# Performance work log

Hardware: AMD Instinct MI355X
Metric: run time of the kernel (lower is better)

Reference implementation:

```python
import jax, jax.numpy as jnp
import numpy as np

K, NC, NA = 9, 13, 5
NB, NH, NW = 128, 26, 26
NT, L = 50, 2 * K + 3
NOOBJ, OBJ, SIL = 1.0, 5.0, 0.6
COORD_S, CLASS_S = 1.0, 1.0
PRETRAIN_EPOCHS = 15
TH, SHARP = 80.0, 2.0                      # corner-conf distance threshold (px), sharpness
SCALE = np.array([640.0, 480.0], np.float32)  # im_width, im_height used by corner_confidences
CONF0 = float(np.exp(SHARP) - 1.0)
ANCHORS = np.array([1.482, 2.2412, 2.0501, 3.1265, 2.3946, 4.6891,
                    3.1018, 3.991, 3.4879, 5.8851], np.float32).reshape(NA, 2)


def setup_inputs():
    k1, k2 = jax.random.split(jax.random.key(0))
    output = jax.random.normal(k1, (NB, NA * (2 * K + 1 + NC), NH, NW), dtype=jnp.float32)
    target = jax.random.uniform(k2, (NB, NT * L), dtype=jnp.float32)
    return {"output": output, "target": target, "epoch": 20}


def _corner_conf(pred, gt):
    # pred, gt: [..., K, 2] normalized corners -> mean per-corner confidence [...]
    d = jnp.sqrt((((pred - gt) * jnp.asarray(SCALE)) ** 2).sum(-1))  # pixel distance [..., K]
    c = (jnp.exp(SHARP * (1.0 - d / TH)) - 1.0) / CONF0
    return jnp.where(d < TH, c, 0.0).mean(-1)


def _region_loss(output, target, epoch):
    nAnch, nPix = NA * NH * NW, NH * NW
    tgt = jax.lax.stop_gradient(target).reshape(NB, NT, L)
    out = output.reshape(NB, NA, 2 * K + 1 + NC, NH, NW)
    # keypoint 0 gets sigmoid, the rest are raw offsets
    xs = jnp.concatenate([jax.nn.sigmoid(out[:, :, 0:1]), out[:, :, 2:2 * K:2]], axis=2)  # [B,A,K,H,W]
    ys = jnp.concatenate([jax.nn.sigmoid(out[:, :, 1:2]), out[:, :, 3:2 * K:2]], axis=2)
    conf = jax.nn.sigmoid(out[:, :, 2 * K])                             # [B,A,H,W]
    cls_logits = jnp.transpose(out[:, :, 2 * K + 1:], (0, 1, 3, 4, 2))  # [B,A,H,W,NC]

    gxg = jnp.arange(NW, dtype=jnp.float32)
    gyg = jnp.arange(NH, dtype=jnp.float32)
    px = (jax.lax.stop_gradient(xs) + gxg) / NW            # detached, as torch uses .data
    py = (jax.lax.stop_gradient(ys) + gyg[:, None]) / NH
    # pred corners per anchor cell, flat anchor index = a*H*W + j*W + i -> [B, A*H*W, K, 2]
    pc = jnp.transpose(jnp.stack([px, py], -1), (0, 1, 3, 4, 2, 5)).reshape(NB, nAnch, K, 2)

    gt_xy = tgt[:, :, 1:1 + 2 * K].reshape(NB, NT, K, 2)
    # torch loop breaks at first target with x1 == 0 -> cumulative validity
    valid = jnp.cumprod((tgt[:, :, 1] != 0).astype(jnp.int32), axis=1) > 0  # [B,T]

    # pass 1: max corner confidence over valid GT, per anchor cell
    def max_conf_step(cur, inp):
        gt_t, v_t = inp                                    # [B,K,2], [B]
        c = _corner_conf(pc, gt_t[:, None]).reshape(NB, NA, NH, NW)
        return jnp.where(v_t[:, None, None, None], jnp.maximum(cur, c), cur), None

    cur_confs, _ = jax.lax.scan(max_conf_step, jnp.zeros((NB, NA, NH, NW), jnp.float32),
                                (jnp.swapaxes(gt_xy, 0, 1), valid.T))
    conf_mask0 = jnp.where(cur_confs > SIL, 0.0, NOOBJ)

    # per-target quantities (vectorized over b,t)
    gx = gt_xy[..., 0] * NW                                # [B,T,K]
    gy = gt_xy[..., 1] * NH
    gi0 = jnp.clip(jnp.floor(gx[:, :, 0]).astype(jnp.int32), 0, NW - 1)  # [B,T]
    gj0 = jnp.clip(jnp.floor(gy[:, :, 0]).astype(jnp.int32), 0, NH - 1)
    # pred_box is fetched with best_n == -1 (as in the source); emulate torch negative flat index via mod
    flat_idx = jnp.mod(jnp.arange(NB)[:, None] * nAnch - nPix + gj0 * NW + gi0, NB * nAnch)
    pred_box = pc.reshape(NB * nAnch, K, 2)[flat_idx]      # [B,T,K,2]
    conf_t = _corner_conf(pred_box, gt_xy)                 # [B,T]
    gw = tgt[:, :, L - 2] * NW
    gh = tgt[:, :, L - 1] * NH
    aw, ah = ANCHORS[:, 0], ANCHORS[:, 1]
    mw = jnp.minimum(aw, gw[..., None])                    # centered-box IoU (bbox_iou, cxcywh)
    mh = jnp.minimum(ah, gh[..., None])
    inter = mw * mh
    iou = inter / (aw * ah + (gw * gh)[..., None] - inter)
    best_n = jnp.argmax(iou, axis=-1).astype(jnp.int32)    # [B,T] (first max, like strict '>')
    txv = gx - gi0[..., None].astype(jnp.float32)          # [B,T,K]
    tyv = gy - gj0[..., None].astype(jnp.float32)
    tclsv = tgt[:, :, 0]

    # pass 2: sequential scatter matching torch overwrite order over t
    barange = jnp.arange(NB)
    z = jnp.zeros((NB, NA, NH, NW), jnp.float32)
    zk = jnp.zeros((NB, NA, NH, NW, K), jnp.float32)

    def scatter_step(carry, inp):
        cm, clm, cfm, tx, ty, tcf, tcl = carry
        v, bn, gj, gi, cft, txt, tyt, tct = inp
        idx = (barange, bn, gj, gi)
        vk = v[:, None]
        cm = cm.at[idx].set(jnp.where(v, 1.0, cm[idx]))
        clm = clm.at[idx].set(jnp.where(v, 1.0, clm[idx]))
        cfm = cfm.at[idx].set(jnp.where(v, OBJ, cfm[idx]))
        tx = tx.at[idx].set(jnp.where(vk, txt, tx[idx]))
        ty = ty.at[idx].set(jnp.where(vk, tyt, ty[idx]))
        tcf = tcf.at[idx].set(jnp.where(v, cft, tcf[idx]))
        tcl = tcl.at[idx].set(jnp.where(v, tct, tcl[idx]))
        return (cm, clm, cfm, tx, ty, tcf, tcl), None

    inps = (valid.T, best_n.T, gj0.T, gi0.T, conf_t.T,
            jnp.swapaxes(txv, 0, 1), jnp.swapaxes(tyv, 0, 1), tclsv.T)
    (coord_mask, cls_mask, conf_mask, tx, ty, tconf, tcls), _ = jax.lax.scan(
        scatter_step, (z, z, conf_mask0, zk, zk, z, z), inps)

    # losses
    xsT = jnp.transpose(xs, (0, 1, 3, 4, 2))               # [B,A,H,W,K]
    ysT = jnp.transpose(ys, (0, 1, 3, 4, 2))
    cmk = coord_mask[..., None]
    loss_x = 0.5 * COORD_S * jnp.sum(((xsT - tx) * cmk) ** 2)
    loss_y = 0.5 * COORD_S * jnp.sum(((ysT - ty) * cmk) ** 2)
    sq = jnp.sqrt(conf_mask)
    loss_conf = 0.5 * jnp.sum(((conf - tconf) * sq) ** 2)
    labels = jnp.clip(tcls.astype(jnp.int32), 0, NC - 1)
    ce = -jnp.take_along_axis(jax.nn.log_softmax(cls_logits, axis=-1),
                              labels[..., None], axis=-1)[..., 0]
    loss_cls = CLASS_S * jnp.sum(ce * cls_mask)
    loss = loss_x + loss_y + loss_cls
    if epoch > PRETRAIN_EPOCHS:
        loss = loss + loss_conf
    return loss


def reference(output, target, epoch):
    return _region_loss(output, target, epoch)
```

## Files before the change

kernel.cpp:

```cpp
#include <hip/hip_runtime.h>
#include <math.h>
#include <stdint.h>

#define KK     9
#define NCLS   13
#define NANC   5
#define NBB    128
#define NHH    26
#define NWW    26
#define NTT    50
#define LL     21
#define CHC    32
#define NPIX   676
#define NANCHT 3380
#define NCELLT 432640
#define GTS    20
#define MWPB   106
#define GTH_W  12
#define NBLKX  53

#define LOG2E_F   1.4426950408889634f
#define K1C       2.8853900817779268f
#define K2C       0.036067376022224085f
#define SXW       24.615384615384617f
#define SYH       18.461538461538463f
#define THRESH_S  43.500902934225507f
#define CONF_T_SCALE 0.017390849194407297f
#define OBJ_W     5.0f
#define EPOCH_PRETRAIN 15
#define BIGV      6.0e18f

#define CULL_H2   0.36f
#define HSCALE    0.03125f

typedef __attribute__((ext_vector_type(2))) float f2;
typedef __attribute__((ext_vector_type(2))) _Float16 h2;
typedef __attribute__((ext_vector_type(4))) unsigned int u4;
typedef __attribute__((ext_vector_type(2))) unsigned int u2;

static __device__ __forceinline__ float fast_exp2(float x){
  return __builtin_amdgcn_exp2f(x);
}
static __device__ __forceinline__ float fast_sqrt(float x){
  return __builtin_amdgcn_sqrtf(x);
}
static __device__ __forceinline__ float sigmoidf_(float x){
  return 1.0f/(1.0f + fast_exp2(-LOG2E_F*x));
}

__constant__ float c_anch[10] = {1.482f,2.2412f,2.0501f,3.1265f,2.3946f,4.6891f,
                                 3.1018f,3.991f,3.4879f,5.8851f};


__global__ __launch_bounds__(64) void prep_kernel(const float* __restrict__ tgt,
                                                  float* __restrict__ gts_neg,
                                                  unsigned int* __restrict__ gth,
                                                  int* __restrict__ nvalid){
  int b = blockIdx.x;
  int t = threadIdx.x;
  const float* trow = tgt + (size_t)b*NTT*LL;
  float v1 = (t < NTT) ? trow[t*LL + 1] : 0.0f;
  unsigned long long mk = __ballot(t < NTT && v1 != 0.0f);
  int firstInvalid = __ffsll(~mk) - 1;
  if (t == 0) nvalid[b] = firstInvalid;
  for (int idx = t; idx < NTT*GTS; idx += 64){
    int tt = idx / GTS;
    int c  = idx - tt*GTS;
    float v;
    if (c == 9 || c == 19)      v = BIGV;
    else if (c < 9)             v = -(trow[tt*LL + 1 + 2*c] * 640.0f);
    else                        v = -(trow[tt*LL + 2 + 2*(c-10)] * 480.0f);
    gts_neg[(size_t)b*NTT*GTS + idx] = v;
  }
  for (int idx = t; idx < NTT*GTH_W; idx += 64){
    int tt = idx / GTH_W;
    int w  = idx - tt*GTH_W;
    const float* tr2 = trow + tt*LL;
    float a0 = BIGV, a1 = BIGV;
    if (w < 5){
      int k0 = 2*w;
      a0 = -(tr2[1 + 2*k0] * 20.0f);
      if (k0 + 1 < KK) a1 = -(tr2[1 + 2*(k0+1)] * 20.0f);
    } else if (w < 10){
      int k0 = 2*(w-5);
      a0 = -(tr2[2 + 2*k0] * 15.0f);
      if (k0 + 1 < KK) a1 = -(tr2[2 + 2*(k0+1)] * 15.0f);
    }
    h2 hh; hh.x = (_Float16)a0; hh.y = (_Float16)a1;
    gth[(size_t)b*NTT*GTH_W + idx] = __builtin_bit_cast(unsigned int, hh);
  }
}

__global__ __launch_bounds__(256) void region_confmask_kernel(
    const float* __restrict__ outp, const float* __restrict__ gts_neg,
    const unsigned int* __restrict__ gth,
    const int* __restrict__ nvalid, unsigned int* __restrict__ maskw,
    double* __restrict__ partials){
  int b    = blockIdx.y;
  int lane = threadIdx.x & 63;
  int w    = threadIdx.x >> 6;
  int cellbase = blockIdx.x * 64;
  int cell = cellbase + lane;
  bool live = (cell < NANCHT);
  int cellc = live ? cell : (NANCHT-1);

  __shared__ unsigned int sgh[NTT*GTH_W] __attribute__((aligned(16)));
  __shared__ float sgt[NTT*GTS] __attribute__((aligned(16)));
  __shared__ unsigned long long sexcl[4];
  {
    const unsigned int* gsrc = gth + (size_t)b*NTT*GTH_W;
    for (int idx = threadIdx.x; idx < NTT*GTH_W; idx += 256) sgh[idx] = gsrc[idx];
    const float* fsrc = gts_neg + (size_t)b*NTT*GTS;
    for (int idx = threadIdx.x; idx < NTT*GTS; idx += 256) sgt[idx] = fsrc[idx];
  }
  __syncthreads();

  int a   = cellc / NPIX;
  int rem = cellc - a*NPIX;
  int j   = rem / NWW;
  int i   = rem - j*NWW;
  const float* base = outp + (((size_t)b*NANC + a)*CHC)*NPIX + rem;

  f2 Pxp[5], Pyp[5];
#pragma unroll
  for (int k = 0; k < KK; ++k){
    float rx = base[(2*k)*NPIX];
    float ry = base[(2*k+1)*NPIX];
    if (k == 0){ rx = sigmoidf_(rx); ry = sigmoidf_(ry); }
    Pxp[k>>1][k&1] = (rx + (float)i) * SXW;
    Pyp[k>>1][k&1] = (ry + (float)j) * SYH;
  }
  Pxp[4][1] = 0.0f; Pyp[4][1] = 0.0f;

  h2 Pxh[5], Pyh[5];
#pragma unroll
  for (int p = 0; p < 5; ++p){
    Pxh[p].x = (_Float16)(Pxp[p].x * HSCALE);
    Pxh[p].y = (_Float16)(Pxp[p].y * HSCALE);
    Pyh[p].x = (_Float16)(Pyp[p].x * HSCALE);
    Pyh[p].y = (_Float16)(Pyp[p].y * HSCALE);
  }

  int nv = nvalid[b];
  int t0 = (w*nv) >> 2;
  int t1 = ((w+1)*nv) >> 2;
  const _Float16 thh = (_Float16)CULL_H2;
  unsigned long long qbits = 0ull;
#pragma unroll 2
  for (int t = t0; t < t1; ++t){
    const u4* q = (const u4*)(sgh + t*GTH_W);
    u4 q0 = q[0];
    u4 q1 = q[1];
    u2 q2 = *(const u2*)(sgh + t*GTH_W + 8);
    h2 Xa[5] = { __builtin_bit_cast(h2, q0.x), __builtin_bit_cast(h2, q0.y),
                 __builtin_bit_cast(h2, q0.z), __builtin_bit_cast(h2, q0.w),
                 __builtin_bit_cast(h2, q1.x) };
    h2 Ya[5] = { __builtin_bit_cast(h2, q1.y), __builtin_bit_cast(h2, q1.z),
                 __builtin_bit_cast(h2, q1.w), __builtin_bit_cast(h2, q2.x),
                 __builtin_bit_cast(h2, q2.y) };
    h2 m2 = {(_Float16)60000.0f, (_Float16)60000.0f};
#pragma unroll
    for (int p = 0; p < 5; ++p){
      h2 dx = Pxh[p] + Xa[p];
      h2 dy = Pyh[p] + Ya[p];
      h2 r  = __builtin_elementwise_fma(dy, dy, dx*dx);
      m2 = __builtin_elementwise_min(m2, r);
    }
    _Float16 mm = (m2.x < m2.y) ? m2.x : m2.y;
    if (mm < thh) qbits |= (1ull << t);
  }

  bool exc = false;
  if (__any(qbits != 0ull)){
    while (qbits){
      int t = __ffsll((long long)qbits) - 1;
      qbits &= qbits - 1;
      const float* gg = sgt + t*GTS;
      float s = 0.0f;
#pragma unroll
      for (int k = 0; k < KK; ++k){
        float dx = Pxp[k>>1][k&1] + gg[k];
        float dy = Pyp[k>>1][k&1] + gg[10+k];
        float d  = fast_sqrt(fmaf(dy, dy, dx*dx));
        float e  = fast_exp2(fmaf(d, -K2C, K1C));
        s += fmaxf(e, 1.0f);
      }
      exc |= (s > THRESH_S);
    }
  }

  unsigned long long em = __ballot(exc);
  if (lane == 0) sexcl[w] = em;
  __syncthreads();

  if (w == 0){
    unsigned long long finalx = sexcl[0] | sexcl[1] | sexcl[2] | sexcl[3];
    int m0 = ((finalx >> lane) & 1ull) ? 0 : 1;

    float cf = sigmoidf_(base[(2*KK)*NPIX]);
    float contrib = (m0 && live) ? 0.5f*cf*cf : 0.0f;

    unsigned long long mb = __ballot(m0 != 0);
    if ((lane & 31) == 0){
      unsigned int wv = (lane == 0) ? (unsigned int)mb : (unsigned int)(mb >> 32);
      maskw[(size_t)b*MWPB + (cellbase >> 5) + (lane >> 5)] = wv;
    }

#pragma unroll
    for (int o = 32; o > 0; o >>= 1) contrib += __shfl_xor(contrib, o, 64);
    if (lane == 0)
      partials[(size_t)b*NBLKX + blockIdx.x] = (double)contrib;
  }
}

__global__ __launch_bounds__(64) void scatter_loss_kernel(
    const float* __restrict__ outp, const float* __restrict__ tgt,
    const int* __restrict__ nvalid, const unsigned int* __restrict__ maskw,
    double* __restrict__ bc_part){
  int b = blockIdx.x;
  int t = threadIdx.x;
  __shared__ int keys[NTT];
  int nv = nvalid[b];
  bool valid = (t < nv);

  int key = -1, gi0 = 0, gj0 = 0, bn = 0;
  float txv[KK], tyv[KK];
  float conf_t = 0.0f, tcls = 0.0f;

  if (t < NTT){
    const float* trow = tgt + ((size_t)b*NTT + t)*LL;
    tcls = trow[0];
    float gx0 = trow[1]*(float)NWW;
    float gy0 = trow[2]*(float)NHH;
    gi0 = min(max((int)floorf(gx0), 0), NWW-1);
    gj0 = min(max((int)floorf(gy0), 0), NHH-1);
#pragma unroll
    for (int k = 0; k < KK; ++k){
      txv[k] = trow[1+2*k]*(float)NWW - (float)gi0;
      tyv[k] = trow[2+2*k]*(float)NHH - (float)gj0;
    }
    float gw = trow[LL-2]*(float)NWW, gh = trow[LL-1]*(float)NHH;
    float best = -1.0f;
    for (int a = 0; a < NANC; ++a){
      float aw = c_anch[2*a], ah = c_anch[2*a+1];
      float inter = fminf(aw, gw) * fminf(ah, gh);
      float iou = inter / (aw*ah + gw*gh - inter);
      if (iou > best){ best = iou; bn = a; }
    }
    key = bn*NPIX + gj0*NWW + gi0;
    keys[t] = key;

    long f = (long)b*NANCHT - NPIX + gj0*NWW + gi0;
    if (f < 0) f += NCELLT;
    int bb  = (int)(f / NANCHT);
    int rr  = (int)(f - (long)bb*NANCHT);
    int aa  = rr / NPIX;
    int rr2 = rr - aa*NPIX;
    int jj  = rr2 / NWW;
    int ii  = rr2 - jj*NWW;
    const float* pbase = outp + (((size_t)bb*NANC + aa)*CHC)*NPIX + rr2;
    float s = 0.0f;
#pragma unroll
    for (int k = 0; k < KK; ++k){
      float rx = pbase[(2*k)*NPIX], ry = pbase[(2*k+1)*NPIX];
      if (k == 0){ rx = sigmoidf_(rx); ry = sigmoidf_(ry); }
      float Pxx = (rx + (float)ii)*SXW, Pyy = (ry + (float)jj)*SYH;
      float dx = Pxx - trow[1+2*k]*640.0f;
      float dy = Pyy - trow[2+2*k]*480.0f;
      float d  = fast_sqrt(fmaf(dy, dy, dx*dx));
      float e  = fast_exp2(fmaf(d, -K2C, K1C));
      s += fmaxf(e, 1.0f);
    }
    conf_t = (s - 9.0f) * CONF_T_SCALE;
  }
  __syncthreads();

  bool winner = valid;
  if (valid){
    for (int u = t+1; u < nv; ++u) if (keys[u] == key){ winner = false; break; }
  }

  double lx = 0.0, ly = 0.0, lcls = 0.0, lcf = 0.0;
  if (winner){
    const float* cbase = outp + (((size_t)b*NANC + bn)*CHC)*NPIX + gj0*NWW + gi0;
    float sx = 0.0f, sy = 0.0f;
#pragma unroll
    for (int k = 0; k < KK; ++k){
      float rx = cbase[(2*k)*NPIX], ry = cbase[(2*k+1)*NPIX];
      if (k == 0){ rx = sigmoidf_(rx); ry = sigmoidf_(ry); }
      float dx = rx - txv[k], dy = ry - tyv[k];
      sx = fmaf(dx, dx, sx); sy = fmaf(dy, dy, sy);
    }
    lx = 0.5*(double)sx; ly = 0.5*(double)sy;

    float lg[NCLS], mx = -1e30f;
#pragma unroll
    for (int c = 0; c < NCLS; ++c){ lg[c] = cbase[(2*KK+1+c)*NPIX]; mx = fmaxf(mx, lg[c]); }
    float se = 0.0f;
#pragma unroll
    for (int c = 0; c < NCLS; ++c) se += fast_exp2((lg[c]-mx)*LOG2E_F);
    int label = min(max((int)tcls, 0), NCLS-1);
    lcls = (double)(mx + logf(se) - lg[label]);

    float cf = sigmoidf_(cbase[(2*KK)*NPIX]);
    int idx = bn*NPIX + gj0*NWW + gi0;
    int m0 = (maskw[(size_t)b*MWPB + (idx >> 5)] >> (idx & 31)) & 1;
    float dcf = cf - conf_t;
    lcf = 0.5*OBJ_W*(double)(dcf*dcf) - (m0 ? 0.5*(double)(cf*cf) : 0.0);
  }

#pragma unroll
  for (int o = 32; o > 0; o >>= 1){
    lx  += __shfl_xor(lx,  o, 64);
    ly  += __shfl_xor(ly,  o, 64);
    lcls+= __shfl_xor(lcls,o, 64);
    lcf += __shfl_xor(lcf, o, 64);
  }
  if (threadIdx.x == 0){
    double* bp = bc_part + (size_t)b*4;
    bp[0] = lx; bp[1] = ly; bp[2] = lcls; bp[3] = lcf;
  }
}

__global__ __launch_bounds__(256) void finalize_kernel(
    const double* __restrict__ bc_part, const double* __restrict__ partials,
    const int* __restrict__ epoch_p, float* __restrict__ outv){
  int tid = threadIdx.x;
  double vx=0, vy=0, vc=0, vf=0, vb=0;
  for (int i = tid; i < NBB; i += 256){
    vx += bc_part[4*i]; vy += bc_part[4*i+1];
    vc += bc_part[4*i+2]; vf += bc_part[4*i+3];
  }
  for (int i = tid; i < NBLKX*NBB; i += 256) vb += partials[i];
#pragma unroll
  for (int o = 32; o > 0; o >>= 1){
    vx += __shfl_xor(vx, o, 64); vy += __shfl_xor(vy, o, 64);
    vc += __shfl_xor(vc, o, 64); vf += __shfl_xor(vf, o, 64);
    vb += __shfl_xor(vb, o, 64);
  }
  __shared__ double sm[5][4];
  int wid = tid >> 6, lane = tid & 63;
  if (lane == 0){ sm[0][wid]=vx; sm[1][wid]=vy; sm[2][wid]=vc; sm[3][wid]=vf; sm[4][wid]=vb; }
  __syncthreads();
  if (tid == 0){
    double fx=0, fy=0, fc=0, ff=0, fb=0;
    for (int w = 0; w < 4; ++w){ fx+=sm[0][w]; fy+=sm[1][w]; fc+=sm[2][w]; ff+=sm[3][w]; fb+=sm[4][w]; }
    double loss = fx + fy + fc;
    if (*epoch_p > EPOCH_PRETRAIN) loss += ff + fb;
    outv[0] = (float)loss;
  }
}

extern "C" void kernel_launch(void* const* d_in, const int* in_sizes, int n_in,
                              void* d_out, int out_size, void* d_ws, size_t ws_size,
                              hipStream_t stream){
  (void)in_sizes; (void)n_in; (void)out_size; (void)ws_size;
  const float* outp = (const float*)d_in[0];
  const float* tgt  = (const float*)d_in[1];
  const int*   ep   = (const int*)d_in[2];
  float* outv = (float*)d_out;
  char* ws = (char*)d_ws;

  double* bc_part  = (double*)(ws);
  double* partials = (double*)(ws + 4096);
  float*  gts_neg  = (float*) (ws + 58368);
  int*    nvalid   = (int*)   (ws + 570368);
  unsigned int* maskw = (unsigned int*)(ws + 570880);
  unsigned int* gth   = (unsigned int*)(ws + 625152);

  prep_kernel<<<dim3(NBB), dim3(64), 0, stream>>>(tgt, gts_neg, gth, nvalid);
  region_confmask_kernel<<<dim3(NBLKX, NBB), dim3(256), 0, stream>>>(outp, gts_neg, gth, nvalid, maskw, partials);
  scatter_loss_kernel<<<dim3(NBB), dim3(64), 0, stream>>>(outp, tgt, nvalid, maskw, bc_part);
  finalize_kernel<<<dim3(1), dim3(256), 0, stream>>>(bc_part, partials, ep, outv);
}
```

Before: 146.3 us.

## Compact culled candidate pairs into shared queue and spread exact checks across block

Prediction corner loads are now split across all four waves by channel and staged in shared memory instead of each wave loading all 18 channels. Candidate (cell, target) pairs passing the fp16 cull are appended to a shared queue with an atomic counter, and the exact fp32 confidence checks are then spread evenly over all 256 threads, with exclusion bits set by shared atomics. This is meant to remove redundant global loads and the divergent per-lane while-loop imbalance, at the cost of extra shared memory, barriers and LDS atomics.

```diff
diff --git a/kernel.cpp b/kernel.cpp
--- a/kernel.cpp
+++ b/kernel.cpp
@@ -18,6 +18,7 @@
 #define MWPB   106
 #define GTH_W  12
 #define NBLKX  53
+#define QMAX   3200
 
 #define LOG2E_F   1.4426950408889634f
 #define K1C       2.8853900817779268f
@@ -46,6 +47,9 @@
 }
 static __device__ __forceinline__ float sigmoidf_(float x){
   return 1.0f/(1.0f + fast_exp2(-LOG2E_F*x));
+}
+static __device__ __forceinline__ h2 cvt_pkrtz_(float a, float b){
+  return __builtin_bit_cast(h2, __builtin_amdgcn_cvt_pkrtz(a, b));
 }
 
 __constant__ float c_anch[10] = {1.482f,2.2412f,2.0501f,3.1265f,2.3946f,4.6891f,
@@ -97,55 +101,69 @@
     const int* __restrict__ nvalid, unsigned int* __restrict__ maskw,
     double* __restrict__ partials){
   int b    = blockIdx.y;
-  int lane = threadIdx.x & 63;
-  int w    = threadIdx.x >> 6;
+  int tid  = threadIdx.x;
+  int lane = tid & 63;
+  int w    = tid >> 6;
   int cellbase = blockIdx.x * 64;
   int cell = cellbase + lane;
   bool live = (cell < NANCHT);
   int cellc = live ? cell : (NANCHT-1);
 
+  __shared__ float sgt[NTT*GTS] __attribute__((aligned(16)));
   __shared__ unsigned int sgh[NTT*GTH_W] __attribute__((aligned(16)));
-  __shared__ float sgt[NTT*GTS] __attribute__((aligned(16)));
-  __shared__ unsigned long long sexcl[4];
+  __shared__ f2 sPx[5*64] __attribute__((aligned(8)));
+  __shared__ f2 sPy[5*64] __attribute__((aligned(8)));
+  __shared__ float sCf[64];
+  __shared__ unsigned short qlist[QMAX];
+  __shared__ int qcount;
+  __shared__ unsigned int sexclw[2];
+
+  if (tid == 0) qcount = 0;
+  if (tid < 2) sexclw[tid] = 0u;
+
   {
+    const float* fsrc = gts_neg + (size_t)b*NTT*GTS;
+    for (int idx = tid; idx < NTT*GTS; idx += 256) sgt[idx] = fsrc[idx];
     const unsigned int* gsrc = gth + (size_t)b*NTT*GTH_W;
-    for (int idx = threadIdx.x; idx < NTT*GTH_W; idx += 256) sgh[idx] = gsrc[idx];
-    const float* fsrc = gts_neg + (size_t)b*NTT*GTS;
-    for (int idx = threadIdx.x; idx < NTT*GTS; idx += 256) sgt[idx] = fsrc[idx];
+    for (int idx = tid; idx < NTT*GTH_W; idx += 256) sgh[idx] = gsrc[idx];
+  }
+
+  {
+    int a   = cellc / NPIX;
+    int rem = cellc - a*NPIX;
+    int jj  = rem / NWW;
+    int ii  = rem - jj*NWW;
+    const float* cb = outp + (((size_t)b*NANC + a)*CHC)*NPIX + rem;
+    for (int ch = w; ch <= 18; ch += 4){
+      float raw = cb[(size_t)ch * NPIX];
+      if (ch == 18){
+        sCf[lane] = sigmoidf_(raw);
+      } else {
+        int k = ch >> 1, axis = ch & 1;
+        float r = (k == 0) ? sigmoidf_(raw) : raw;
+        float v = axis ? (r + (float)jj) * SYH : (r + (float)ii) * SXW;
+        float* dst = axis ? (float*)sPy : (float*)sPx;
+        dst[(((k >> 1)*64) + lane)*2 + (k & 1)] = v;
+      }
+    }
   }
   __syncthreads();
 
-  int a   = cellc / NPIX;
-  int rem = cellc - a*NPIX;
-  int j   = rem / NWW;
-  int i   = rem - j*NWW;
-  const float* base = outp + (((size_t)b*NANC + a)*CHC)*NPIX + rem;
-
-  f2 Pxp[5], Pyp[5];
-#pragma unroll
-  for (int k = 0; k < KK; ++k){
-    float rx = base[(2*k)*NPIX];
-    float ry = base[(2*k+1)*NPIX];
-    if (k == 0){ rx = sigmoidf_(rx); ry = sigmoidf_(ry); }
-    Pxp[k>>1][k&1] = (rx + (float)i) * SXW;
-    Pyp[k>>1][k&1] = (ry + (float)j) * SYH;
-  }
-  Pxp[4][1] = 0.0f; Pyp[4][1] = 0.0f;
-
   h2 Pxh[5], Pyh[5];
 #pragma unroll
   for (int p = 0; p < 5; ++p){
-    Pxh[p].x = (_Float16)(Pxp[p].x * HSCALE);
-    Pxh[p].y = (_Float16)(Pxp[p].y * HSCALE);
-    Pyh[p].x = (_Float16)(Pyp[p].x * HSCALE);
-    Pyh[p].y = (_Float16)(Pyp[p].y * HSCALE);
+    f2 px = sPx[p*64 + lane];
+    f2 py = sPy[p*64 + lane];
+    if (p == 4){ px.y = 0.0f; py.y = 0.0f; }
+    px *= HSCALE; py *= HSCALE;
+    Pxh[p] = cvt_pkrtz_(px.x, px.y);
+    Pyh[p] = cvt_pkrtz_(py.x, py.y);
   }
 
   int nv = nvalid[b];
   int t0 = (w*nv) >> 2;
   int t1 = ((w+1)*nv) >> 2;
   const _Float16 thh = (_Float16)CULL_H2;
-  unsigned long long qbits = 0ull;
 #pragma unroll 2
   for (int t = t0; t < t1; ++t){
     const u4* q = (const u4*)(sgh + t*GTH_W);
@@ -167,37 +185,47 @@
       m2 = __builtin_elementwise_min(m2, r);
     }
     _Float16 mm = (m2.x < m2.y) ? m2.x : m2.y;
-    if (mm < thh) qbits |= (1ull << t);
-  }
-
-  bool exc = false;
-  if (__any(qbits != 0ull)){
-    while (qbits){
-      int t = __ffsll((long long)qbits) - 1;
-      qbits &= qbits - 1;
-      const float* gg = sgt + t*GTS;
-      float s = 0.0f;
-#pragma unroll
-      for (int k = 0; k < KK; ++k){
-        float dx = Pxp[k>>1][k&1] + gg[k];
-        float dy = Pyp[k>>1][k&1] + gg[10+k];
+    if (mm < thh){
+      int qi = atomicAdd(&qcount, 1);
+      qlist[qi] = (unsigned short)(lane | (t << 6));
+    }
+  }
+  __syncthreads();
+
+  int n = qcount;
+  for (int idx = tid; idx < n; idx += 256){
+    unsigned int pkid = qlist[idx];
+    int l2 = pkid & 63;
+    int t  = pkid >> 6;
+    const float* gg = sgt + t*GTS;
+    float s = 0.0f;
+#pragma unroll
+    for (int p = 0; p < 5; ++p){
+      f2 px = sPx[p*64 + l2];
+      f2 py = sPy[p*64 + l2];
+      {
+        float dx = px.x + gg[2*p];
+        float dy = py.x + gg[10 + 2*p];
         float d  = fast_sqrt(fmaf(dy, dy, dx*dx));
         float e  = fast_exp2(fmaf(d, -K2C, K1C));
         s += fmaxf(e, 1.0f);
       }
-      exc |= (s > THRESH_S);
-    }
-  }
-
-  unsigned long long em = __ballot(exc);
-  if (lane == 0) sexcl[w] = em;
+      if (p < 4){
+        float dx = px.y + gg[2*p + 1];
+        float dy = py.y + gg[10 + 2*p + 1];
+        float d  = fast_sqrt(fmaf(dy, dy, dx*dx));
+        float e  = fast_exp2(fmaf(d, -K2C, K1C));
+        s += fmaxf(e, 1.0f);
+      }
+    }
+    if (s > THRESH_S) atomicOr(&sexclw[l2 >> 5], 1u << (l2 & 31));
+  }
   __syncthreads();
 
   if (w == 0){
-    unsigned long long finalx = sexcl[0] | sexcl[1] | sexcl[2] | sexcl[3];
-    int m0 = ((finalx >> lane) & 1ull) ? 0 : 1;
-
-    float cf = sigmoidf_(base[(2*KK)*NPIX]);
+    unsigned int ex = sexclw[lane >> 5];
+    int m0 = ((ex >> (lane & 31)) & 1u) ? 0 : 1;
+    float cf = sCf[lane];
     float contrib = (m0 && live) ? 0.5f*cf*cf : 0.0f;
 
     unsigned long long mb = __ballot(m0 != 0);
```

Measured after the change: 145.2 us. Within noise of the previous version (-0.8%).

## Give each wave two cells over all targets instead of splitting targets across waves

Applied to the files above, without the earlier changes.

Before, each block covered 64 cells and its four waves split the target list, then merged the results through shared memory. Now each block covers 512 cells: every wave owns two 64-cell groups and loops over all valid targets, reusing each shared-memory target load for both cells. This cuts the grid from 53 to 7 blocks per batch, so the per-block shared-memory staging is amortized over more cells and the cross-wave OR merge goes away. In exchange, register pressure rises because each thread holds two cells' corners, and there are fewer blocks for latency hiding.

```diff
diff --git a/kernel.cpp b/kernel.cpp
--- a/kernel.cpp
+++ b/kernel.cpp
@@ -17,7 +17,7 @@
 #define GTS    20
 #define MWPB   106
 #define GTH_W  12
-#define NBLKX  53
+#define NBLKX  7
 
 #define LOG2E_F   1.4426950408889634f
 #define K1C       2.8853900817779268f
@@ -97,57 +97,81 @@
     const int* __restrict__ nvalid, unsigned int* __restrict__ maskw,
     double* __restrict__ partials){
   int b    = blockIdx.y;
-  int lane = threadIdx.x & 63;
-  int w    = threadIdx.x >> 6;
-  int cellbase = blockIdx.x * 64;
-  int cell = cellbase + lane;
-  bool live = (cell < NANCHT);
-  int cellc = live ? cell : (NANCHT-1);
-
+  int tid  = threadIdx.x;
+  int lane = tid & 63;
+  int w    = tid >> 6;
+  int waveA = blockIdx.x * 512 + w*64;
+  int waveB = waveA + 256;
+  int cA = waveA + lane;
+  int cB = waveB + lane;
+  bool liveA = (cA < NANCHT);
+  bool liveB = (cB < NANCHT);
+  int cAc = liveA ? cA : (NANCHT-1);
+  int cBc = liveB ? cB : (NANCHT-1);
+
+  __shared__ float sgt[NTT*GTS] __attribute__((aligned(16)));
   __shared__ unsigned int sgh[NTT*GTH_W] __attribute__((aligned(16)));
-  __shared__ float sgt[NTT*GTS] __attribute__((aligned(16)));
-  __shared__ unsigned long long sexcl[4];
   {
+    const float* fsrc = gts_neg + (size_t)b*NTT*GTS;
+    for (int idx = tid; idx < NTT*GTS; idx += 256) sgt[idx] = fsrc[idx];
     const unsigned int* gsrc = gth + (size_t)b*NTT*GTH_W;
-    for (int idx = threadIdx.x; idx < NTT*GTH_W; idx += 256) sgh[idx] = gsrc[idx];
-    const float* fsrc = gts_neg + (size_t)b*NTT*GTS;
-    for (int idx = threadIdx.x; idx < NTT*GTS; idx += 256) sgt[idx] = fsrc[idx];
+    for (int idx = tid; idx < NTT*GTH_W; idx += 256) sgh[idx] = gsrc[idx];
   }
   __syncthreads();
 
-  int a   = cellc / NPIX;
-  int rem = cellc - a*NPIX;
-  int j   = rem / NWW;
-  int i   = rem - j*NWW;
-  const float* base = outp + (((size_t)b*NANC + a)*CHC)*NPIX + rem;
-
-  f2 Pxp[5], Pyp[5];
-#pragma unroll
-  for (int k = 0; k < KK; ++k){
-    float rx = base[(2*k)*NPIX];
-    float ry = base[(2*k+1)*NPIX];
-    if (k == 0){ rx = sigmoidf_(rx); ry = sigmoidf_(ry); }
-    Pxp[k>>1][k&1] = (rx + (float)i) * SXW;
-    Pyp[k>>1][k&1] = (ry + (float)j) * SYH;
-  }
-  Pxp[4][1] = 0.0f; Pyp[4][1] = 0.0f;
-
-  h2 Pxh[5], Pyh[5];
+  f2 PxpA[5], PypA[5], PxpB[5], PypB[5];
+  h2 PxhA[5], PyhA[5], PxhB[5], PyhB[5];
+  const float* baseA;
+  const float* baseB;
+  {
+    int a   = cAc / NPIX;
+    int rem = cAc - a*NPIX;
+    int j   = rem / NWW;
+    int i   = rem - j*NWW;
+    baseA = outp + (((size_t)b*NANC + a)*CHC)*NPIX + rem;
+#pragma unroll
+    for (int k = 0; k < KK; ++k){
+      float rx = baseA[(2*k)*NPIX];
+      float ry = baseA[(2*k+1)*NPIX];
+      if (k == 0){ rx = sigmoidf_(rx); ry = sigmoidf_(ry); }
+      PxpA[k>>1][k&1] = (rx + (float)i) * SXW;
+      PypA[k>>1][k&1] = (ry + (float)j) * SYH;
+    }
+    PxpA[4][1] = 0.0f; PypA[4][1] = 0.0f;
+  }
+  {
+    int a   = cBc / NPIX;
+    int rem = cBc - a*NPIX;
+    int j   = rem / NWW;
+    int i   = rem - j*NWW;
+    baseB = outp + (((size_t)b*NANC + a)*CHC)*NPIX + rem;
+#pragma unroll
+    for (int k = 0; k < KK; ++k){
+      float rx = baseB[(2*k)*NPIX];
+      float ry = baseB[(2*k+1)*NPIX];
+      if (k == 0){ rx = sigmoidf_(rx); ry = sigmoidf_(ry); }
+      PxpB[k>>1][k&1] = (rx + (float)i) * SXW;
+      PypB[k>>1][k&1] = (ry + (float)j) * SYH;
+    }
+    PxpB[4][1] = 0.0f; PypB[4][1] = 0.0f;
+  }
 #pragma unroll
   for (int p = 0; p < 5; ++p){
-    Pxh[p].x = (_Float16)(Pxp[p].x * HSCALE);
-    Pxh[p].y = (_Float16)(Pxp[p].y * HSCALE);
-    Pyh[p].x = (_Float16)(Pyp[p].x * HSCALE);
-    Pyh[p].y = (_Float16)(Pyp[p].y * HSCALE);
+    PxhA[p].x = (_Float16)(PxpA[p].x * HSCALE);
+    PxhA[p].y = (_Float16)(PxpA[p].y * HSCALE);
+    PyhA[p].x = (_Float16)(PypA[p].x * HSCALE);
+    PyhA[p].y = (_Float16)(PypA[p].y * HSCALE);
+    PxhB[p].x = (_Float16)(PxpB[p].x * HSCALE);
+    PxhB[p].y = (_Float16)(PxpB[p].y * HSCALE);
+    PyhB[p].x = (_Float16)(PypB[p].x * HSCALE);
+    PyhB[p].y = (_Float16)(PypB[p].y * HSCALE);
   }
 
   int nv = nvalid[b];
-  int t0 = (w*nv) >> 2;
-  int t1 = ((w+1)*nv) >> 2;
   const _Float16 thh = (_Float16)CULL_H2;
-  unsigned long long qbits = 0ull;
+  unsigned long long qbitsA = 0ull, qbitsB = 0ull;
 #pragma unroll 2
-  for (int t = t0; t < t1; ++t){
+  for (int t = 0; t < nv; ++t){
     const u4* q = (const u4*)(sgh + t*GTH_W);
     u4 q0 = q[0];
     u4 q1 = q[1];
@@ -158,58 +182,89 @@
     h2 Ya[5] = { __builtin_bit_cast(h2, q1.y), __builtin_bit_cast(h2, q1.z),
                  __builtin_bit_cast(h2, q1.w), __builtin_bit_cast(h2, q2.x),
                  __builtin_bit_cast(h2, q2.y) };
-    h2 m2 = {(_Float16)60000.0f, (_Float16)60000.0f};
+    h2 m2A = {(_Float16)60000.0f, (_Float16)60000.0f};
+    h2 m2B = {(_Float16)60000.0f, (_Float16)60000.0f};
 #pragma unroll
     for (int p = 0; p < 5; ++p){
-      h2 dx = Pxh[p] + Xa[p];
-      h2 dy = Pyh[p] + Ya[p];
-      h2 r  = __builtin_elementwise_fma(dy, dy, dx*dx);
-      m2 = __builtin_elementwise_min(m2, r);
-    }
-    _Float16 mm = (m2.x < m2.y) ? m2.x : m2.y;
-    if (mm < thh) qbits |= (1ull << t);
-  }
-
-  bool exc = false;
-  if (__any(qbits != 0ull)){
-    while (qbits){
-      int t = __ffsll((long long)qbits) - 1;
-      qbits &= qbits - 1;
+      h2 dxA = PxhA[p] + Xa[p];
+      h2 dyA = PyhA[p] + Ya[p];
+      h2 rA  = __builtin_elementwise_fma(dyA, dyA, dxA*dxA);
+      m2A = __builtin_elementwise_min(m2A, rA);
+      h2 dxB = PxhB[p] + Xa[p];
+      h2 dyB = PyhB[p] + Ya[p];
+      h2 rB  = __builtin_elementwise_fma(dyB, dyB, dxB*dxB);
+      m2B = __builtin_elementwise_min(m2B, rB);
+    }
+    _Float16 mmA = (m2A.x < m2A.y) ? m2A.x : m2A.y;
+    _Float16 mmB = (m2B.x < m2B.y) ? m2B.x : m2B.y;
+    if (mmA < thh) qbitsA |= (1ull << t);
+    if (mmB < thh) qbitsB |= (1ull << t);
+  }
+
+  int m0A = 1, m0B = 1;
+  if (__any((qbitsA | qbitsB) != 0ull)){
+    bool excA = false, excB = false;
+    while (qbitsA){
+      int t = __ffsll((long long)qbitsA) - 1;
+      qbitsA &= qbitsA - 1;
       const float* gg = sgt + t*GTS;
       float s = 0.0f;
 #pragma unroll
       for (int k = 0; k < KK; ++k){
-        float dx = Pxp[k>>1][k&1] + gg[k];
-        float dy = Pyp[k>>1][k&1] + gg[10+k];
+        float dx = PxpA[k>>1][k&1] + gg[k];
+        float dy = PypA[k>>1][k&1] + gg[10+k];
         float d  = fast_sqrt(fmaf(dy, dy, dx*dx));
         float e  = fast_exp2(fmaf(d, -K2C, K1C));
         s += fmaxf(e, 1.0f);
       }
-      exc |= (s > THRESH_S);
-    }
-  }
-
-  unsigned long long em = __ballot(exc);
-  if (lane == 0) sexcl[w] = em;
+      excA |= (s > THRESH_S);
+    }
+    while (qbitsB){
+      int t = __ffsll((long long)qbitsB) - 1;
+      qbitsB &= qbitsB - 1;
+      const float* gg = sgt + t*GTS;
+      float s = 0.0f;
+#pragma unroll
+      for (int k = 0; k < KK; ++k){
+        float dx = PxpB[k>>1][k&1] + gg[k];
+        float dy = PypB[k>>1][k&1] + gg[10+k];
+        float d  = fast_sqrt(fmaf(dy, dy, dx*dx));
+        float e  = fast_exp2(fmaf(d, -K2C, K1C));
+        s += fmaxf(e, 1.0f);
+      }
+      excB |= (s > THRESH_S);
+    }
+    if (excA) m0A = 0;
+    if (excB) m0B = 0;
+  }
+
+  float cfA = sigmoidf_(baseA[(2*KK)*NPIX]);
+  float cfB = sigmoidf_(baseB[(2*KK)*NPIX]);
+  float contrib = ((m0A && liveA) ? 0.5f*cfA*cfA : 0.0f)
+                + ((m0B && liveB) ? 0.5f*cfB*cfB : 0.0f);
+
+  unsigned long long mbA = __ballot(m0A != 0);
+  unsigned long long mbB = __ballot(m0B != 0);
+  if ((lane & 31) == 0){
+    if (waveA < NANCHT){
+      unsigned int wv = (lane == 0) ? (unsigned int)mbA : (unsigned int)(mbA >> 32);
+      maskw[(size_t)b*MWPB + (waveA >> 5) + (lane >> 5)] = wv;
+    }
+    if (waveB < NANCHT){
+      unsigned int wv = (lane == 0) ? (unsigned int)mbB : (unsigned int)(mbB >> 32);
+      maskw[(size_t)b*MWPB + (waveB >> 5) + (lane >> 5)] = wv;
+    }
+  }
+
+#pragma unroll
+  for (int o = 32; o > 0; o >>= 1) contrib += __shfl_xor(contrib, o, 64);
+  __shared__ float wsum[4];
+  int wid = tid >> 6;
+  if (lane == 0) wsum[wid] = contrib;
   __syncthreads();
-
-  if (w == 0){
-    unsigned long long finalx = sexcl[0] | sexcl[1] | sexcl[2] | sexcl[3];
-    int m0 = ((finalx >> lane) & 1ull) ? 0 : 1;
-
-    float cf = sigmoidf_(base[(2*KK)*NPIX]);
-    float contrib = (m0 && live) ? 0.5f*cf*cf : 0.0f;
-
-    unsigned long long mb = __ballot(m0 != 0);
-    if ((lane & 31) == 0){
-      unsigned int wv = (lane == 0) ? (unsigned int)mb : (unsigned int)(mb >> 32);
-      maskw[(size_t)b*MWPB + (cellbase >> 5) + (lane >> 5)] = wv;
-    }
-
-#pragma unroll
-    for (int o = 32; o > 0; o >>= 1) contrib += __shfl_xor(contrib, o, 64);
-    if (lane == 0)
-      partials[(size_t)b*NBLKX + blockIdx.x] = (double)contrib;
+  if (tid == 0){
+    double tot = (double)wsum[0] + (double)wsum[1] + (double)wsum[2] + (double)wsum[3];
+    partials[blockIdx.y * gridDim.x + blockIdx.x] = tot;
   }
 }
 
@@ -363,10 +418,10 @@
 
   double* bc_part  = (double*)(ws);
   double* partials = (double*)(ws + 4096);
-  float*  gts_neg  = (float*) (ws + 58368);
-  int*    nvalid   = (int*)   (ws + 570368);
-  unsigned int* maskw = (unsigned int*)(ws + 570880);
-  unsigned int* gth   = (unsigned int*)(ws + 625152);
+  float*  gts_neg  = (float*) (ws + 18432);
+  int*    nvalid   = (int*)   (ws + 530432);
+  unsigned int* maskw = (unsigned int*)(ws + 530944);
+  unsigned int* gth   = (unsigned int*)(ws + 585216);
 
   prep_kernel<<<dim3(NBB), dim3(64), 0, stream>>>(tgt, gts_neg, gth, nvalid);
   region_confmask_kernel<<<dim3(NBLKX, NBB), dim3(256), 0, stream>>>(outp, gts_neg, gth, nvalid, maskw, partials);
```

Result: faster. 141.8 us (-3.1%).
